# Performance work log

Hardware: AMD Instinct MI355X
Metric: run time of the kernel (lower is better)

## Reference

```python
import jax, jax.numpy as jnp
import numpy as np

V, C, H = 4096, 512, 8
D = C // H
EPS = 1e-5


def setup_inputs():
    key = jax.random.key(0)
    ks = jax.random.split(key, 8)
    s = 0.02
    f32 = jnp.float32
    return {
        "z": jax.random.normal(ks[0], (4, C, 1024), f32),
        "q": 256,
        "codebook": jax.random.normal(ks[1], (V, C), f32) * s,
        "Wq": jax.random.normal(ks[2], (C, C), f32) * s,
        "bq": jnp.zeros((C,), f32),
        "Wk": jax.random.normal(ks[3], (C, C), f32) * s,
        "bk": jnp.zeros((C,), f32),
        "Wv": jax.random.normal(ks[4], (C, C), f32) * s,
        "bv": jnp.zeros((C,), f32),
        "Wp": jax.random.normal(ks[5], (C, H), f32) * s,
        "bp": jnp.zeros((H,), f32),
        "gq": jnp.ones((D,), f32),
        "gk": jnp.ones((D,), f32),
    }


def _rmsnorm(x, g):
    return x * jax.lax.rsqrt(jnp.mean(x * x, axis=-1, keepdims=True) + EPS) * g


def _attn_logits(hs_bct, codebook, Wq, bq, Wk, bk, Wp, bp, gq, gk):
    # pooled cross-attention logits over codebook entries: (B,N,T)
    B, Cc, T = hs_bct.shape
    hs = hs_bct.transpose(0, 2, 1)  # (B,T,C)
    qh = (hs @ Wq + bq).reshape(B, T, H, D).transpose(0, 2, 1, 3)  # (B,H,T,D)
    kh = (codebook @ Wk + bk).reshape(-1, H, D).transpose(1, 0, 2)  # (H,N,D)
    c = hs @ Wp + bp  # (B,T,H) head-pooling weights
    qh = _rmsnorm(qh, gq)
    kh = _rmsnorm(kh, gk)
    logits = jnp.einsum('bhtd,hnd->bhnt', qh, kh) * (1.0 / float(np.sqrt(D)))
    logits = jnp.einsum('bth,bhnt->bnt', c, logits) * (1.0 / float(np.sqrt(H)))
    return logits


def _linear_interp(x, T):
    # x: (B,C,q) -> (B,C,T); matches F.interpolate(mode='linear', align_corners=False)
    q = x.shape[-1]
    pos = (jnp.arange(T, dtype=x.dtype) + 0.5) * (q / T) - 0.5
    pos = jnp.clip(pos, 0.0, q - 1.0)
    i0 = jnp.floor(pos).astype(jnp.int32)
    i1 = jnp.minimum(i0 + 1, q - 1)
    w = (pos - i0.astype(x.dtype))
    return x[..., i0] * (1.0 - w) + x[..., i1] * w


def reference(z, q, codebook, Wq, bq, Wk, bk, Wv, bv, Wp, bp, gq, gk):
    B, Cc, T = z.shape
    # area interpolation T -> q (T % q == 0): non-overlapping window mean
    rest = z.reshape(B, Cc, q, T // q).mean(-1) if q != T else z  # (B,C,q)
    logits = _attn_logits(rest, codebook, Wq, bq, Wk, bk, Wp, bp, gq, gk)  # (B,V,q)
    soft = jax.nn.softmax(logits, axis=1)
    code_idx = jnp.argmax(soft, axis=1)  # (B,q)
    hard = jax.nn.one_hot(code_idx, V, dtype=logits.dtype).transpose(0, 2, 1)  # (B,V,q)
    one_hot = hard - jax.lax.stop_gradient(soft) + soft  # straight-through
    value = codebook @ Wv + bv  # (V,C)
    z_hat = jnp.einsum('bnt,nd->bdt', one_hot, value)  # (B,C,q)
    z_hat = _linear_interp(z_hat, T)  # (B,C,T); phi == identity
    # full-resolution index pass (torch.no_grad) for perplexity (eval path)
    logits_org = jax.lax.stop_gradient(
        _attn_logits(z, codebook, Wq, bq, Wk, bk, Wp, bp, gq, gk))
    code_org = jnp.argmax(logits_org, axis=1).reshape(-1)  # (B*T,)
    counts = jnp.zeros((V,), jnp.float32).at[code_org].add(1.0)
    prob = counts / counts.sum()
    perplexity = jnp.exp(-jnp.sum(prob * jnp.log(prob + 1e-7)))
    return z_hat, perplexity
```

## Files before the change

### kernel.cpp

```cpp
#include <hip/hip_runtime.h>
#include <hip/hip_bf16.h>
#include <cfloat>
#include <math.h>

#define NFULL 4096
#define NPOOL 1024
#define NTOK  5120
#define VDIM  4096

typedef __attribute__((ext_vector_type(8))) short short8;
typedef __attribute__((ext_vector_type(4))) float f4;
typedef unsigned long long u64;

#define MFMA16(a,b,c) __builtin_amdgcn_mfma_f32_16x16x32_bf16((a),(b),(c),0,0,0)

static __device__ __forceinline__ void gl_lds16(const void* g, void* l) {
    __builtin_amdgcn_global_load_lds(
        (const __attribute__((address_space(1))) unsigned int*)g,
        (__attribute__((address_space(3))) unsigned int*)l, 16, 0, 0);
}

#define BGEMM3_CORE(AM, Bt)                                                    \
    int lane = tid & 63, w = tid >> 6, wy = w >> 1, wx = w & 1;                \
    int lm = lane & 15, quad = lane >> 4;                                      \
    int lr8 = lane >> 3;                                                       \
    int kcs = (lane & 7) ^ lr8;                                                \
    int rS = w * 32 + lr8;                                                     \
    const __hip_bfloat16* Ag = (AM) + (mB + rS) * 512 + kcs * 8;               \
    const __hip_bfloat16* Bg = (Bt) + (nB + rS) * 512 + kcs * 8;               \
    __hip_bfloat16* Al = As + (w * 32) * 64 + lane * 8;                        \
    __hip_bfloat16* Bl = Bs + (w * 32) * 64 + lane * 8;                        \
    f4 acc[4][4];                                                              \
    _Pragma("unroll") for (int i = 0; i < 4; ++i)                              \
        _Pragma("unroll") for (int j = 0; j < 4; ++j)                          \
            acc[i][j] = f4{0.f, 0.f, 0.f, 0.f};                                \
    int aswz = lm & 7;                                                         \
    for (int kt = 0; kt < 8; ++kt) {                                           \
        __syncthreads();                                                       \
        _Pragma("unroll") for (int i = 0; i < 4; ++i) {                        \
            gl_lds16(Ag + kt * 64 + i * 8 * 512, Al + i * 8 * 64);             \
            gl_lds16(Bg + kt * 64 + i * 8 * 512, Bl + i * 8 * 64);             \
        }                                                                      \
        __syncthreads();                                                       \
        _Pragma("unroll") for (int s = 0; s < 2; ++s) {                        \
            short8 aF[4], bF[4];                                               \
            int slot = ((s * 4 + quad) ^ aswz) << 3;                           \
            _Pragma("unroll") for (int mt = 0; mt < 4; ++mt)                   \
                aF[mt] = *(const short8*)(As + (wy * 64 + mt * 16 + lm) * 64 + slot); \
            _Pragma("unroll") for (int nt = 0; nt < 4; ++nt)                   \
                bF[nt] = *(const short8*)(Bs + (wx * 64 + nt * 16 + lm) * 64 + slot); \
            _Pragma("unroll") for (int mt = 0; mt < 4; ++mt)                   \
                _Pragma("unroll") for (int nt = 0; nt < 4; ++nt)               \
                    acc[mt][nt] = MFMA16(aF[mt], bF[nt], acc[mt][nt]);         \
        }                                                                      \
    }

__global__ void prep_k(const float* __restrict__ z, const float* __restrict__ cbk,
                       const float* __restrict__ Wq, const float* __restrict__ Wv,
                       float* __restrict__ X, __hip_bfloat16* __restrict__ Xh,
                       __hip_bfloat16* __restrict__ cbh,
                       __hip_bfloat16* __restrict__ WqT, __hip_bfloat16* __restrict__ WvT,
                       u64* __restrict__ packed, unsigned int* __restrict__ Kmax2i) {
    __shared__ float smem[33 * 32];
    int bx = blockIdx.x;
    if (bx < 2048) {
        float (*tile)[33] = (float(*)[33])smem;
        int t0 = (bx & 31) * 32, c0 = ((bx >> 5) & 15) * 32, b = bx >> 9;
        int tx = threadIdx.x & 31, ty = threadIdx.x >> 5;
        #pragma unroll
        for (int i = 0; i < 4; ++i) {
            int c = ty + i * 8;
            tile[c][tx] = z[((b << 9) + c0 + c) * 1024 + t0 + tx];
        }
        __syncthreads();
        #pragma unroll
        for (int i = 0; i < 4; ++i) {
            int tl = ty + i * 8;
            int tok = (b << 10) + t0 + tl;
            Xh[tok * 512 + c0 + tx] = __float2bfloat16(tile[tx][tl]);
        }
        float m = 0.25f * (tile[tx][ty * 4] + tile[tx][ty * 4 + 1] +
                           tile[tx][ty * 4 + 2] + tile[tx][ty * 4 + 3]);
        int tq = (t0 >> 2) + ty;
        X[(NFULL + (b << 8) + tq) * 512 + c0 + tx] = m;
    } else if (bx < 4096) {
        int i0 = (bx - 2048) * 1024 + threadIdx.x * 4;
        float4 v = *(const float4*)(cbk + i0);
        __hip_bfloat16* d = cbh + i0;
        d[0] = __float2bfloat16(v.x); d[1] = __float2bfloat16(v.y);
        d[2] = __float2bfloat16(v.z); d[3] = __float2bfloat16(v.w);
    } else if (bx < 4608) {
        int lin = bx - 4096;
        const float* W = (lin >> 8) ? Wv : Wq;
        __hip_bfloat16* WT = (lin >> 8) ? WvT : WqT;
        float (*t)[33] = (float(*)[33])smem;
        int bk = ((lin >> 4) & 15) * 32, bn = (lin & 15) * 32;
        int lx = threadIdx.x & 31, ly = threadIdx.x >> 5;
        #pragma unroll
        for (int i = 0; i < 4; ++i) {
            int r = ly * 4 + i;
            t[r][lx] = W[(bk + r) * 512 + bn + lx];
        }
        __syncthreads();
        #pragma unroll
        for (int i = 0; i < 4; ++i) {
            int r = ly * 4 + i;
            WT[(bn + r) * 512 + bk + lx] = __float2bfloat16(t[lx][r]);
        }
    } else {
        int i = (bx - 4608) * 256 + threadIdx.x;
        packed[i] = 0ull;
        if (bx == 4608 && threadIdx.x == 0) Kmax2i[0] = 0u;
    }
}

__global__ __launch_bounds__(256) void mid1_k(
    const __hip_bfloat16* __restrict__ Xh,
    const float* __restrict__ cbk, const float* __restrict__ Xp,
    const float* __restrict__ Wk, const float* __restrict__ Wq,
    const float* __restrict__ Wp, const float* __restrict__ bp,
    float* __restrict__ P0, float* __restrict__ P1, float* __restrict__ Cp) {
    __shared__ __align__(16) char smraw[16640];
    int bx = blockIdx.x, tid = threadIdx.x;
    if (bx < 640) {
        float (*As2)[68]  = (float(*)[68])smraw;
        float (*Bs2)[132] = (float(*)[132])(smraw + 16 * 68 * 4);
        int kz = bx >= 320;
        int rem = bx - kz * 320;
        int mB = (rem % 80) * 64, nB = (rem / 80) * 128, kOff = kz * 256;
        const float *A, *B;
        if (mB < NFULL) { A = cbk + mB * 512; B = Wk; }
        else            { A = Xp + (mB - NFULL) * 512; B = Wq; }
        int ty = tid >> 4, tx = tid & 15;
        int arow = tid >> 2, achk = tid & 3;
        int brow = tid >> 4, bcol = (tid & 15) * 4;
        const float* Ap = A + arow * 512 + kOff + achk * 4;
        const float* Bp = B + (kOff + brow) * 512 + nB + bcol;
        float acc[4][8] = {};
        for (int kt = 0; kt < 16; ++kt) {
            float4 a  = *(const float4*)(Ap + kt * 16);
            float4 b0 = *(const float4*)(Bp + kt * 16 * 512);
            float4 b1 = *(const float4*)(Bp + kt * 16 * 512 + 64);
            __syncthreads();
            As2[achk * 4 + 0][arow] = a.x; As2[achk * 4 + 1][arow] = a.y;
            As2[achk * 4 + 2][arow] = a.z; As2[achk * 4 + 3][arow] = a.w;
            *(float4*)&Bs2[brow][bcol]      = b0;
            *(float4*)&Bs2[brow][bcol + 64] = b1;
            __syncthreads();
            #pragma unroll
            for (int kk = 0; kk < 16; ++kk) {
                float4 av  = *(const float4*)&As2[kk][ty * 4];
                float4 bv0 = *(const float4*)&Bs2[kk][tx * 4];
                float4 bv1 = *(const float4*)&Bs2[kk][64 + tx * 4];
                float a4[4] = {av.x, av.y, av.z, av.w};
                float b8[8] = {bv0.x, bv0.y, bv0.z, bv0.w, bv1.x, bv1.y, bv1.z, bv1.w};
                #pragma unroll
                for (int i = 0; i < 4; ++i)
                    #pragma unroll
                    for (int j = 0; j < 8; ++j)
                        acc[i][j] = fmaf(a4[i], b8[j], acc[i][j]);
            }
        }
        float* P = kz ? P1 : P0;
        #pragma unroll
        for (int i = 0; i < 4; ++i) {
            int row = mB + ty * 4 + i;
            float4 r0, r1;
            r0.x = acc[i][0]; r0.y = acc[i][1]; r0.z = acc[i][2]; r0.w = acc[i][3];
            r1.x = acc[i][4]; r1.y = acc[i][5]; r1.z = acc[i][6]; r1.w = acc[i][7];
            *(float4*)&P[row * 512 + nB + tx * 4]      = r0;
            *(float4*)&P[row * 512 + nB + 64 + tx * 4] = r1;
        }
    } else {
        float* Wl = (float*)smraw;
        for (int i = tid; i < 4096; i += 256) Wl[i + (i >> 6)] = Wp[i];
        __syncthreads();
        int w = tid >> 6, lane = tid & 63;
        int tok = (bx - 640) * 4 + w;
        float x[8];
        if (tok < NFULL) {
            short8 xv = *(const short8*)(Xh + tok * 512 + lane * 8);
            #pragma unroll
            for (int j = 0; j < 8; ++j)
                x[j] = __uint_as_float(((unsigned)(unsigned short)xv[j]) << 16);
        } else {
            const float* xp = Xp + (tok - NFULL) * 512 + lane * 8;
            float4 a = *(const float4*)xp, b = *(const float4*)(xp + 4);
            x[0] = a.x; x[1] = a.y; x[2] = a.z; x[3] = a.w;
            x[4] = b.x; x[5] = b.y; x[6] = b.z; x[7] = b.w;
        }
        float s[8] = {};
        int base = lane * 65;
        #pragma unroll
        for (int j = 0; j < 8; ++j)
            #pragma unroll
            for (int h = 0; h < 8; ++h)
                s[h] = fmaf(x[j], Wl[base + j * 8 + h], s[h]);
        #pragma unroll
        for (int h = 0; h < 8; ++h)
            #pragma unroll
            for (int o = 32; o > 0; o >>= 1) s[h] += __shfl_xor(s[h], o);
        if (lane == 0) {
            #pragma unroll
            for (int h = 0; h < 8; ++h) Cp[tok * 8 + h] = s[h] + bp[h];
        }
    }
}

__global__ __launch_bounds__(256) void mid2_k(
    const __hip_bfloat16* __restrict__ Xh, const __hip_bfloat16* __restrict__ WqT,
    const __hip_bfloat16* __restrict__ cbh, const __hip_bfloat16* __restrict__ WvT,
    const float* __restrict__ P0, const float* __restrict__ P1,
    const float* __restrict__ bk, const float* __restrict__ bq,
    const float* __restrict__ gk, const float* __restrict__ gq,
    const float* __restrict__ Cp, const float* __restrict__ bvv,
    __hip_bfloat16* __restrict__ Qh, float* __restrict__ Vb,
    float* __restrict__ Kn, __hip_bfloat16* __restrict__ Kh,
    float* __restrict__ Qpool, unsigned int* __restrict__ Kmax2i) {
    __shared__ __align__(16) char smraw[32768];
    int bx = blockIdx.x, tid = threadIdx.x;
    if (bx < 256) {
        int part = bx >> 7, rem = bx & 127;
        int mB = (rem & 31) * 128, nB = (rem >> 5) * 128;
        const __hip_bfloat16* AM = part ? cbh : Xh;
        const __hip_bfloat16* Bt = part ? WvT : WqT;
        __hip_bfloat16* As = (__hip_bfloat16*)smraw;
        __hip_bfloat16* Bs = As + 128 * 64;
        BGEMM3_CORE(AM, Bt)
        if (part == 0) {
            int h = (rem >> 5) * 2 + wx;
            float bb[4], gg[4];
            #pragma unroll
            for (int nt = 0; nt < 4; ++nt) {
                bb[nt] = bq[h * 64 + nt * 16 + lm];
                gg[nt] = gq[nt * 16 + lm];
            }
            #pragma unroll
            for (int mt = 0; mt < 4; ++mt)
                #pragma unroll
                for (int reg = 0; reg < 4; ++reg) {
                    int tok = mB + wy * 64 + mt * 16 + quad * 4 + reg;
                    float vv[4], ss = 0.f;
                    #pragma unroll
                    for (int nt = 0; nt < 4; ++nt) {
                        vv[nt] = acc[mt][nt][reg] + bb[nt];
                        ss = fmaf(vv[nt], vv[nt], ss);
                    }
                    #pragma unroll
                    for (int off = 1; off < 16; off <<= 1) ss += __shfl_xor(ss, off);
                    float sc = rsqrtf(ss * (1.0f / 64.0f) + 1e-5f) *
                               Cp[tok * 8 + h] * 0.04419417382415922f;
                    #pragma unroll
                    for (int nt = 0; nt < 4; ++nt)
                        Qh[tok * 512 + h * 64 + nt * 16 + lm] =
                            __float2bfloat16(vv[nt] * sc * gg[nt]);
                }
        } else {
            float bb[4];
            #pragma unroll
            for (int nt = 0; nt < 4; ++nt) bb[nt] = bvv[nB + wx * 64 + nt * 16 + lm];
            #pragma unroll
            for (int mt = 0; mt < 4; ++mt)
                #pragma unroll
                for (int reg = 0; reg < 4; ++reg) {
                    int m = mB + wy * 64 + mt * 16 + quad * 4 + reg;
                    #pragma unroll
                    for (int nt = 0; nt < 4; ++nt)
                        Vb[m * 512 + nB + wx * 64 + nt * 16 + lm] =
                            acc[mt][nt][reg] + bb[nt];
                }
        }
    } else {
        int w = tid >> 6, lane = tid & 63;
        int row = (bx - 256) * 4 + w;
        bool isQ = row >= NFULL;
        const float* bias = isQ ? bq : bk;
        const float* g = isQ ? gq : gk;
        int c0 = lane * 8;
        const float* p0 = P0 + row * 512 + c0;
        const float* p1 = P1 + row * 512 + c0;
        float4 a0 = *(const float4*)p0,  a1 = *(const float4*)(p0 + 4);
        float4 d0 = *(const float4*)p1,  d1 = *(const float4*)(p1 + 4);
        float4 e0 = *(const float4*)(bias + c0), e1 = *(const float4*)(bias + c0 + 4);
        int gi = (lane & 7) * 8;
        float4 g0 = *(const float4*)(g + gi), g1 = *(const float4*)(g + gi + 4);
        float v[8];
        v[0] = a0.x + d0.x + e0.x; v[1] = a0.y + d0.y + e0.y;
        v[2] = a0.z + d0.z + e0.z; v[3] = a0.w + d0.w + e0.w;
        v[4] = a1.x + d1.x + e1.x; v[5] = a1.y + d1.y + e1.y;
        v[6] = a1.z + d1.z + e1.z; v[7] = a1.w + d1.w + e1.w;
        float ss = 0.f;
        #pragma unroll
        for (int j = 0; j < 8; ++j) ss = fmaf(v[j], v[j], ss);
        ss += __shfl_xor(ss, 1); ss += __shfl_xor(ss, 2); ss += __shfl_xor(ss, 4);
        float sc = rsqrtf(ss * (1.0f / 64.0f) + 1e-5f);
        float gg[8] = {g0.x, g0.y, g0.z, g0.w, g1.x, g1.y, g1.z, g1.w};
        float o_[8];
        #pragma unroll
        for (int j = 0; j < 8; ++j) o_[j] = v[j] * sc * gg[j];
        if (isQ) {
            float cf = Cp[row * 8 + (lane >> 3)] * 0.04419417382415922f;
            #pragma unroll
            for (int j = 0; j < 8; ++j) o_[j] *= cf;
            float* qp = Qpool + (row - NFULL) * 512 + c0;
            *(float4*)qp       = make_float4(o_[0], o_[1], o_[2], o_[3]);
            *(float4*)(qp + 4) = make_float4(o_[4], o_[5], o_[6], o_[7]);
            __hip_bfloat16 hb[8];
            #pragma unroll
            for (int j = 0; j < 8; ++j) hb[j] = __float2bfloat16(o_[j]);
            *(short8*)(Qh + row * 512 + c0) = *(const short8*)hb;
        } else {
            float* kp = Kn + row * 512 + c0;
            *(float4*)kp       = make_float4(o_[0], o_[1], o_[2], o_[3]);
            *(float4*)(kp + 4) = make_float4(o_[4], o_[5], o_[6], o_[7]);
            __hip_bfloat16 hb[8];
            #pragma unroll
            for (int j = 0; j < 8; ++j) hb[j] = __float2bfloat16(o_[j]);
            *(short8*)(Kh + row * 512 + c0) = *(const short8*)hb;
            float rs = 0.f;
            #pragma unroll
            for (int j = 0; j < 8; ++j) rs = fmaf(o_[j], o_[j], rs);
            #pragma unroll
            for (int o = 32; o > 0; o >>= 1) rs += __shfl_xor(rs, o);
            float* wsum = (float*)smraw;
            if (lane == 0) wsum[w] = rs;
            __syncthreads();
            if (tid == 0) {
                float m01 = fmaxf(wsum[0], wsum[1]);
                float m23 = fmaxf(wsum[2], wsum[3]);
                atomicMax(Kmax2i, __float_as_uint(fmaxf(m01, m23)));
            }
        }
    }
}

__global__ __launch_bounds__(512, 4) void logits_full_k(
    const __hip_bfloat16* __restrict__ Qh, const __hip_bfloat16* __restrict__ Kh,
    u64* __restrict__ packed, __hip_bfloat16* __restrict__ Lp) {
    __shared__ __hip_bfloat16 As[128 * 64];
    __shared__ __hip_bfloat16 Bs[256 * 64];
    int tid = threadIdx.x;
    int mB = blockIdx.x * 128, nB = blockIdx.y * 256;
    int lane = tid & 63, w = tid >> 6;
    int wy = w >> 2, wx = w & 3;
    int lm = lane & 15, quad = lane >> 4;
    int lr8 = lane >> 3;
    int kcs = (lane & 7) ^ lr8;
    const __hip_bfloat16* Ag = Qh + (mB + w * 16 + lr8) * 512 + kcs * 8;
    const __hip_bfloat16* Bg = Kh + (nB + w * 32 + lr8) * 512 + kcs * 8;
    __hip_bfloat16* Al = As + (w * 16) * 64 + lane * 8;
    __hip_bfloat16* Bl = Bs + (w * 32) * 64 + lane * 8;
    f4 acc[4][4];
    #pragma unroll
    for (int i = 0; i < 4; ++i)
        #pragma unroll
        for (int j = 0; j < 4; ++j) acc[i][j] = f4{0.f, 0.f, 0.f, 0.f};
    int aswz = lm & 7;
    for (int kt = 0; kt < 8; ++kt) {
        __syncthreads();
        #pragma unroll
        for (int i = 0; i < 2; ++i)
            gl_lds16(Ag + kt * 64 + i * 8 * 512, Al + i * 8 * 64);
        #pragma unroll
        for (int i = 0; i < 4; ++i)
            gl_lds16(Bg + kt * 64 + i * 8 * 512, Bl + i * 8 * 64);
        __syncthreads();
        #pragma unroll
        for (int s = 0; s < 2; ++s) {
            short8 aF[4], bF[4];
            int slot = ((s * 4 + quad) ^ aswz) << 3;
            #pragma unroll
            for (int mt = 0; mt < 4; ++mt)
                aF[mt] = *(const short8*)(As + (wy * 64 + mt * 16 + lm) * 64 + slot);
            #pragma unroll
            for (int nt = 0; nt < 4; ++nt)
                bF[nt] = *(const short8*)(Bs + (wx * 64 + nt * 16 + lm) * 64 + slot);
            #pragma unroll
            for (int mt = 0; mt < 4; ++mt)
                #pragma unroll
                for (int nt = 0; nt < 4; ++nt)
                    acc[mt][nt] = MFMA16(aF[mt], bF[nt], acc[mt][nt]);
        }
    }
    if (blockIdx.x < 32) {
        #pragma unroll
        for (int mt = 0; mt < 4; ++mt)
            #pragma unroll
            for (int reg = 0; reg < 4; ++reg) {
                float bv = -FLT_MAX; int bi = 0;
                #pragma unroll
                for (int nt = 0; nt < 4; ++nt) {
                    float v = acc[mt][nt][reg];
                    int n = nB + wx * 64 + nt * 16 + lm;
                    if (v > bv) { bv = v; bi = n; }
                }
                #pragma unroll
                for (int off = 1; off < 16; off <<= 1) {
                    float ov = __shfl_xor(bv, off);
                    int oi = __shfl_xor(bi, off);
                    if (ov > bv || (ov == bv && oi < bi)) { bv = ov; bi = oi; }
                }
                if (lm == 0) {
                    unsigned ub = __float_as_uint(bv);
                    ub = (ub & 0x80000000u) ? ~ub : (ub | 0x80000000u);
                    u64 key = ((u64)ub << 32) | (u64)(0xFFFFFFFFu - (unsigned)bi);
                    int tok = mB + wy * 64 + mt * 16 + quad * 4 + reg;
                    atomicMax(&packed[tok], key);
                }
            }
    } else {
        #pragma unroll
        for (int mt = 0; mt < 4; ++mt)
            #pragma unroll
            for (int reg = 0; reg < 4; ++reg) {
                int tok = mB + wy * 64 + mt * 16 + quad * 4 + reg;
                long long base = (long long)(tok - NFULL) * 4096;
                #pragma unroll
                for (int nt = 0; nt < 4; ++nt)
                    Lp[base + nB + wx * 64 + nt * 16 + lm] =
                        __float2bfloat16(acc[mt][nt][reg]);
            }
    }
}

__global__ __launch_bounds__(256) void tail_k(
    const float* __restrict__ Qpool, const float* __restrict__ Kn,
    const __hip_bfloat16* __restrict__ Lp, const unsigned int* __restrict__ Kmax2i,
    const u64* __restrict__ packed, int* __restrict__ codeP,
    float* __restrict__ outPpl) {
    __shared__ int cnt[4096];
    __shared__ float red[4];
    int tid = threadIdx.x;
    if (blockIdx.x < 256) {
        int wid = tid >> 6, lane = tid & 63;
        int tok = blockIdx.x * 4 + wid;
        const float* q = Qpool + tok * 512;
        float4 q0 = *(const float4*)(q + lane * 8);
        float4 q1 = *(const float4*)(q + lane * 8 + 4);
        float qs = q0.x * q0.x + q0.y * q0.y + q0.z * q0.z + q0.w * q0.w +
                   q1.x * q1.x + q1.y * q1.y + q1.z * q1.z + q1.w * q1.w;
        #pragma unroll
        for (int o = 32; o > 0; o >>= 1) qs += __shfl_xor(qs, o);
        float delta = 0.0078125f * sqrtf(qs) * sqrtf(__uint_as_float(*Kmax2i));
        const __hip_bfloat16* row = Lp + (long long)tok * 4096;
        float mx = -FLT_MAX;
        for (int c = 0; c < 64; ++c)
            mx = fmaxf(mx, __bfloat162float(row[c * 64 + lane]));
        #pragma unroll
        for (int o = 32; o > 0; o >>= 1) mx = fmaxf(mx, __shfl_xor(mx, o));
        float thr = mx - delta;
        float bv = -FLT_MAX; int bi = 0;
        for (int c = 0; c < 64; ++c) {
            float v = __bfloat162float(row[c * 64 + lane]);
            u64 mask = __ballot(v >= thr);
            while (mask) {
                int l = __ffsll((long long)mask) - 1;
                mask &= mask - 1;
                int n = c * 64 + l;
                const float* k = Kn + n * 512;
                float4 k0 = *(const float4*)(k + lane * 8);
                float4 k1 = *(const float4*)(k + lane * 8 + 4);
                float d = q0.x * k0.x;
                d = fmaf(q0.y, k0.y, d); d = fmaf(q0.z, k0.z, d); d = fmaf(q0.w, k0.w, d);
                d = fmaf(q1.x, k1.x, d); d = fmaf(q1.y, k1.y, d);
                d = fmaf(q1.z, k1.z, d); d = fmaf(q1.w, k1.w, d);
                #pragma unroll
                for (int o = 32; o > 0; o >>= 1) d += __shfl_xor(d, o);
                if (d > bv) { bv = d; bi = n; }
            }
        }
        if (lane == 0) codeP[tok] = bi;
    } else {
        for (int i = tid; i < 4096; i += 256) cnt[i] = 0;
        __syncthreads();
        for (int i = tid; i < 4096; i += 256) {
            int bi = (int)(0xFFFFFFFFu - (unsigned)(packed[i] & 0xFFFFFFFFu));
            atomicAdd(&cnt[bi], 1);
        }
        __syncthreads();
        float s = 0.f;
        for (int i = tid; i < 4096; i += 256) {
            float p = (float)cnt[i] * (1.0f / 4096.0f);
            s += p * logf(p + 1e-7f);
        }
        #pragma unroll
        for (int o = 32; o > 0; o >>= 1) s += __shfl_xor(s, o);
        if ((tid & 63) == 0) red[tid >> 6] = s;
        __syncthreads();
        if (tid == 0)
            outPpl[0] = expf(-(red[0] + red[1] + red[2] + red[3]));
    }
}

__global__ void zhat_k(const float* __restrict__ Vv, const int* __restrict__ codeP,
                       float* __restrict__ out) {
    int w = (blockIdx.x << 2) + (threadIdx.x >> 6);
    int lane = threadIdx.x & 63;
    int b = w >> 8, j = w & 255;
    const int* cb = codeP + (b << 8);
    const float* rm = Vv + cb[max(j - 1, 0)] * 512;
    const float* r0 = Vv + cb[j] * 512;
    const float* rp = Vv + cb[min(j + 1, 255)] * 512;
    #pragma unroll
    for (int i = 0; i < 8; ++i) {
        int c = i * 64 + lane;
        float vm = rm[c], v0 = r0[c], vp = rp[c];
        float4 o;
        o.x = 0.375f * vm + 0.625f * v0;
        o.y = 0.125f * vm + 0.875f * v0;
        o.z = 0.875f * v0 + 0.125f * vp;
        o.w = 0.625f * v0 + 0.375f * vp;
        *(float4*)&out[(((b << 9) + c) << 10) + (j << 2)] = o;
    }
}

extern "C" void kernel_launch(void* const* d_in, const int* in_sizes, int n_in,
                              void* d_out, int out_size, void* d_ws, size_t ws_size,
                              hipStream_t stream) {
    const float* z   = (const float*)d_in[0];
    const float* cbk = (const float*)d_in[2];
    const float* Wq  = (const float*)d_in[3];
    const float* bq  = (const float*)d_in[4];
    const float* Wk  = (const float*)d_in[5];
    const float* bk  = (const float*)d_in[6];
    const float* Wv  = (const float*)d_in[7];
    const float* bv  = (const float*)d_in[8];
    const float* Wp  = (const float*)d_in[9];
    const float* bp  = (const float*)d_in[10];
    const float* gq  = (const float*)d_in[11];
    const float* gk  = (const float*)d_in[12];
    float* out = (float*)d_out;

    float* X      = (float*)d_ws;
    float* Qpool  = X + 5120 * 512;
    float* Kn     = Qpool + 1024 * 512;
    float* Vb     = Kn + 4096 * 512;
    float* Cp     = Vb + 4096 * 512;
    float* P0     = Cp + 5120 * 8;
    float* P1     = P0 + 5120 * 512;
    u64*   packed = (u64*)(P1 + 5120 * 512);
    unsigned int* Kmax2i = (unsigned int*)(packed + 4096);
    int*   codeP  = (int*)(Kmax2i + 4);
    __hip_bfloat16* Qh  = (__hip_bfloat16*)(codeP + 1024);
    __hip_bfloat16* Kh  = Qh + 5120 * 512;
    __hip_bfloat16* Xh  = Kh + 4096 * 512;
    __hip_bfloat16* cbh = Xh + 4096 * 512;
    __hip_bfloat16* WqT = cbh + 4096 * 512;
    __hip_bfloat16* WvT = WqT + 512 * 512;
    __hip_bfloat16* Lp  = (__hip_bfloat16*)P0;

    prep_k<<<4624, 256, 0, stream>>>(z, cbk, Wq, Wv, X, Xh, cbh, WqT, WvT,
                                     packed, Kmax2i);
    mid1_k<<<1920, 256, 0, stream>>>(Xh, cbk, X + 4096 * 512, Wk, Wq, Wp, bp,
                                     P0, P1, Cp);
    mid2_k<<<1536, 256, 0, stream>>>(Xh, WqT, cbh, WvT, P0, P1, bk, bq, gk, gq,
                                     Cp, bv, Qh, Vb, Kn, Kh, Qpool, Kmax2i);
    logits_full_k<<<dim3(40, 16), 512, 0, stream>>>(Qh, Kh, packed, Lp);
    tail_k<<<257, 256, 0, stream>>>(Qpool, Kn, Lp, Kmax2i, packed, codeP,
                                    out + 4 * 512 * 1024);
    zhat_k<<<256, 256, 0, stream>>>(Vb, codeP, out);
}
```

Measured before the change: 223.7 us.

## Split codebook K projection four ways along K and prefetch tiles in mid1

The fp32 codebook@Wk GEMM in mid1_k moves from a 2-way to a 4-way split-K, so more blocks run with shorter K loops. The extra partials go into reused workspace (Kn and X), and mid2_k adds them back in. The main loop also now register-prefetches the next A/B tile while the current one is computed. The aim is better GPU occupancy and hiding global-load latency, at the cost of extra partial-sum traffic and aliasing risk on the reused buffers: mid2_k reads P2 from Kn and writes Kn in the same rows, and P3 aliases X.

```diff
diff --git a/kernel.cpp b/kernel.cpp
--- a/kernel.cpp
+++ b/kernel.cpp
@@ -119,34 +119,51 @@
     const float* __restrict__ cbk, const float* __restrict__ Xp,
     const float* __restrict__ Wk, const float* __restrict__ Wq,
     const float* __restrict__ Wp, const float* __restrict__ bp,
-    float* __restrict__ P0, float* __restrict__ P1, float* __restrict__ Cp) {
+    float* __restrict__ P0, float* __restrict__ P1,
+    float* __restrict__ P2, float* __restrict__ P3,
+    float* __restrict__ Cp) {
     __shared__ __align__(16) char smraw[16640];
     int bx = blockIdx.x, tid = threadIdx.x;
-    if (bx < 640) {
+    if (bx < 1152) {
         float (*As2)[68]  = (float(*)[68])smraw;
         float (*Bs2)[132] = (float(*)[132])(smraw + 16 * 68 * 4);
-        int kz = bx >= 320;
-        int rem = bx - kz * 320;
-        int mB = (rem % 80) * 64, nB = (rem / 80) * 128, kOff = kz * 256;
-        const float *A, *B;
-        if (mB < NFULL) { A = cbk + mB * 512; B = Wk; }
-        else            { A = Xp + (mB - NFULL) * 512; B = Wq; }
+        const float *A, *B; float* P;
+        int mB, nB, kOff, nkt;
+        if (bx < 1024) {
+            int part = bx >> 8, rem = bx & 255;
+            mB = (rem & 63) * 64; nB = (rem >> 6) * 128;
+            kOff = part * 128; nkt = 8;
+            A = cbk + mB * 512; B = Wk;
+            P = (part == 0) ? P0 : (part == 1) ? P1 : (part == 2) ? P2 : P3;
+        } else {
+            int lin = bx - 1024;
+            int part = lin >> 6, rem = lin & 63;
+            mB = NFULL + (rem & 15) * 64; nB = (rem >> 4) * 128;
+            kOff = part * 256; nkt = 16;
+            A = Xp + (rem & 15) * 64 * 512; B = Wq;
+            P = part ? P1 : P0;
+        }
         int ty = tid >> 4, tx = tid & 15;
         int arow = tid >> 2, achk = tid & 3;
         int brow = tid >> 4, bcol = (tid & 15) * 4;
         const float* Ap = A + arow * 512 + kOff + achk * 4;
         const float* Bp = B + (kOff + brow) * 512 + nB + bcol;
         float acc[4][8] = {};
-        for (int kt = 0; kt < 16; ++kt) {
-            float4 a  = *(const float4*)(Ap + kt * 16);
-            float4 b0 = *(const float4*)(Bp + kt * 16 * 512);
-            float4 b1 = *(const float4*)(Bp + kt * 16 * 512 + 64);
+        float4 a  = *(const float4*)(Ap);
+        float4 b0 = *(const float4*)(Bp);
+        float4 b1 = *(const float4*)(Bp + 64);
+        for (int kt = 0; kt < nkt; ++kt) {
             __syncthreads();
             As2[achk * 4 + 0][arow] = a.x; As2[achk * 4 + 1][arow] = a.y;
             As2[achk * 4 + 2][arow] = a.z; As2[achk * 4 + 3][arow] = a.w;
             *(float4*)&Bs2[brow][bcol]      = b0;
             *(float4*)&Bs2[brow][bcol + 64] = b1;
             __syncthreads();
+            if (kt + 1 < nkt) {
+                a  = *(const float4*)(Ap + (kt + 1) * 16);
+                b0 = *(const float4*)(Bp + (kt + 1) * 16 * 512);
+                b1 = *(const float4*)(Bp + (kt + 1) * 16 * 512 + 64);
+            }
             #pragma unroll
             for (int kk = 0; kk < 16; ++kk) {
                 float4 av  = *(const float4*)&As2[kk][ty * 4];
@@ -161,7 +178,6 @@
                         acc[i][j] = fmaf(a4[i], b8[j], acc[i][j]);
             }
         }
-        float* P = kz ? P1 : P0;
         #pragma unroll
         for (int i = 0; i < 4; ++i) {
             int row = mB + ty * 4 + i;
@@ -176,7 +192,7 @@
         for (int i = tid; i < 4096; i += 256) Wl[i + (i >> 6)] = Wp[i];
         __syncthreads();
         int w = tid >> 6, lane = tid & 63;
-        int tok = (bx - 640) * 4 + w;
+        int tok = (bx - 1152) * 4 + w;
         float x[8];
         if (tok < NFULL) {
             short8 xv = *(const short8*)(Xh + tok * 512 + lane * 8);
@@ -211,11 +227,12 @@
     const __hip_bfloat16* __restrict__ Xh, const __hip_bfloat16* __restrict__ WqT,
     const __hip_bfloat16* __restrict__ cbh, const __hip_bfloat16* __restrict__ WvT,
     const float* __restrict__ P0, const float* __restrict__ P1,
+    const float* P2, const float* __restrict__ P3,
     const float* __restrict__ bk, const float* __restrict__ bq,
     const float* __restrict__ gk, const float* __restrict__ gq,
     const float* __restrict__ Cp, const float* __restrict__ bvv,
     __hip_bfloat16* __restrict__ Qh, float* __restrict__ Vb,
-    float* __restrict__ Kn, __hip_bfloat16* __restrict__ Kh,
+    float* Kn, __hip_bfloat16* __restrict__ Kh,
     float* __restrict__ Qpool, unsigned int* __restrict__ Kmax2i) {
     __shared__ __align__(16) char smraw[32768];
     int bx = blockIdx.x, tid = threadIdx.x;
@@ -289,6 +306,16 @@
         v[2] = a0.z + d0.z + e0.z; v[3] = a0.w + d0.w + e0.w;
         v[4] = a1.x + d1.x + e1.x; v[5] = a1.y + d1.y + e1.y;
         v[6] = a1.z + d1.z + e1.z; v[7] = a1.w + d1.w + e1.w;
+        if (!isQ) {
+            const float* p2 = P2 + row * 512 + c0;
+            const float* p3 = P3 + row * 512 + c0;
+            float4 x0 = *(const float4*)p2, x1 = *(const float4*)(p2 + 4);
+            float4 y0 = *(const float4*)p3, y1 = *(const float4*)(p3 + 4);
+            v[0] += x0.x + y0.x; v[1] += x0.y + y0.y;
+            v[2] += x0.z + y0.z; v[3] += x0.w + y0.w;
+            v[4] += x1.x + y1.x; v[5] += x1.y + y1.y;
+            v[6] += x1.z + y1.z; v[7] += x1.w + y1.w;
+        }
         float ss = 0.f;
         #pragma unroll
         for (int j = 0; j < 8; ++j) ss = fmaf(v[j], v[j], ss);
@@ -548,13 +575,16 @@
     __hip_bfloat16* WqT = cbh + 4096 * 512;
     __hip_bfloat16* WvT = WqT + 512 * 512;
     __hip_bfloat16* Lp  = (__hip_bfloat16*)P0;
+    float* P2 = Kn;
+    float* P3 = X;
 
     prep_k<<<4624, 256, 0, stream>>>(z, cbk, Wq, Wv, X, Xh, cbh, WqT, WvT,
                                      packed, Kmax2i);
-    mid1_k<<<1920, 256, 0, stream>>>(Xh, cbk, X + 4096 * 512, Wk, Wq, Wp, bp,
-                                     P0, P1, Cp);
-    mid2_k<<<1536, 256, 0, stream>>>(Xh, WqT, cbh, WvT, P0, P1, bk, bq, gk, gq,
-                                     Cp, bv, Qh, Vb, Kn, Kh, Qpool, Kmax2i);
+    mid1_k<<<2432, 256, 0, stream>>>(Xh, cbk, X + 4096 * 512, Wk, Wq, Wp, bp,
+                                     P0, P1, P2, P3, Cp);
+    mid2_k<<<1536, 256, 0, stream>>>(Xh, WqT, cbh, WvT, P0, P1, P2, P3,
+                                     bk, bq, gk, gq, Cp, bv,
+                                     Qh, Vb, Kn, Kh, Qpool, Kmax2i);
     logits_full_k<<<dim3(40, 16), 512, 0, stream>>>(Qh, Kh, packed, Lp);
     tail_k<<<257, 256, 0, stream>>>(Qpool, Kn, Lp, Kmax2i, packed, codeP,
                                     out + 4 * 512 * 1024);
```

New measurement: 221.7 us, median of 2. No clear change (-0.9%).

## Replace FP32 SIMT K/Q projection GEMMs with split-bf16 MFMA three-term products

Applied to the files above, without the earlier changes.

The codebook@Wk and pooled-X@Wq projections move from a scalar FP32 FMA GEMM split over K to bf16 MFMA GEMMs. Each FP32 operand is split into bf16 high and low parts, and three partial products (hi*hi, hi*lo, lo*hi) approximate FP32 accuracy. The prep kernel now also writes the hi/lo split and transposed copies of the codebook, pooled X, Wk and Wq. The consumer sums three partial buffers instead of two, which adds extra conversion traffic and a third partial-sum read in exchange for tensor-core throughput.

```diff
diff --git a/kernel.cpp b/kernel.cpp
--- a/kernel.cpp
+++ b/kernel.cpp
@@ -57,9 +57,13 @@
 
 __global__ void prep_k(const float* __restrict__ z, const float* __restrict__ cbk,
                        const float* __restrict__ Wq, const float* __restrict__ Wv,
+                       const float* __restrict__ Wk,
                        float* __restrict__ X, __hip_bfloat16* __restrict__ Xh,
-                       __hip_bfloat16* __restrict__ cbh,
-                       __hip_bfloat16* __restrict__ WqT, __hip_bfloat16* __restrict__ WvT,
+                       __hip_bfloat16* __restrict__ cbh, __hip_bfloat16* __restrict__ cbl,
+                       __hip_bfloat16* __restrict__ Xph, __hip_bfloat16* __restrict__ Xpl,
+                       __hip_bfloat16* __restrict__ WqT, __hip_bfloat16* __restrict__ WqTl,
+                       __hip_bfloat16* __restrict__ WvT,
+                       __hip_bfloat16* __restrict__ WkTh, __hip_bfloat16* __restrict__ WkTl,
                        u64* __restrict__ packed, unsigned int* __restrict__ Kmax2i) {
     __shared__ float smem[33 * 32];
     int bx = blockIdx.x;
@@ -82,17 +86,27 @@
         float m = 0.25f * (tile[tx][ty * 4] + tile[tx][ty * 4 + 1] +
                            tile[tx][ty * 4 + 2] + tile[tx][ty * 4 + 3]);
         int tq = (t0 >> 2) + ty;
-        X[(NFULL + (b << 8) + tq) * 512 + c0 + tx] = m;
+        int prow = (b << 8) + tq;
+        X[(NFULL + prow) * 512 + c0 + tx] = m;
+        __hip_bfloat16 mh = __float2bfloat16(m);
+        Xph[prow * 512 + c0 + tx] = mh;
+        Xpl[prow * 512 + c0 + tx] = __float2bfloat16(m - __bfloat162float(mh));
     } else if (bx < 4096) {
         int i0 = (bx - 2048) * 1024 + threadIdx.x * 4;
         float4 v = *(const float4*)(cbk + i0);
         __hip_bfloat16* d = cbh + i0;
-        d[0] = __float2bfloat16(v.x); d[1] = __float2bfloat16(v.y);
-        d[2] = __float2bfloat16(v.z); d[3] = __float2bfloat16(v.w);
-    } else if (bx < 4608) {
+        __hip_bfloat16* dl = cbl + i0;
+        float vv[4] = {v.x, v.y, v.z, v.w};
+        #pragma unroll
+        for (int j = 0; j < 4; ++j) {
+            __hip_bfloat16 h = __float2bfloat16(vv[j]);
+            d[j] = h;
+            dl[j] = __float2bfloat16(vv[j] - __bfloat162float(h));
+        }
+    } else if (bx < 4864) {
         int lin = bx - 4096;
-        const float* W = (lin >> 8) ? Wv : Wq;
-        __hip_bfloat16* WT = (lin >> 8) ? WvT : WqT;
+        int sel = lin >> 8;
+        const float* W = (sel == 0) ? Wq : (sel == 1) ? Wv : Wk;
         float (*t)[33] = (float(*)[33])smem;
         int bk = ((lin >> 4) & 15) * 32, bn = (lin & 15) * 32;
         int lx = threadIdx.x & 31, ly = threadIdx.x >> 5;
@@ -105,78 +119,74 @@
         #pragma unroll
         for (int i = 0; i < 4; ++i) {
             int r = ly * 4 + i;
-            WT[(bn + r) * 512 + bk + lx] = __float2bfloat16(t[lx][r]);
+            float v = t[lx][r];
+            int idx = (bn + r) * 512 + bk + lx;
+            __hip_bfloat16 h = __float2bfloat16(v);
+            if (sel == 0) {
+                WqT[idx] = h;
+                WqTl[idx] = __float2bfloat16(v - __bfloat162float(h));
+            } else if (sel == 1) {
+                WvT[idx] = h;
+            } else {
+                WkTh[idx] = h;
+                WkTl[idx] = __float2bfloat16(v - __bfloat162float(h));
+            }
         }
     } else {
-        int i = (bx - 4608) * 256 + threadIdx.x;
+        int i = (bx - 4864) * 256 + threadIdx.x;
         packed[i] = 0ull;
-        if (bx == 4608 && threadIdx.x == 0) Kmax2i[0] = 0u;
+        if (bx == 4864 && threadIdx.x == 0) Kmax2i[0] = 0u;
     }
 }
 
 __global__ __launch_bounds__(256) void mid1_k(
     const __hip_bfloat16* __restrict__ Xh,
-    const float* __restrict__ cbk, const float* __restrict__ Xp,
-    const float* __restrict__ Wk, const float* __restrict__ Wq,
+    const __hip_bfloat16* __restrict__ cbh, const __hip_bfloat16* __restrict__ cbl,
+    const __hip_bfloat16* __restrict__ Xph, const __hip_bfloat16* __restrict__ Xpl,
+    const __hip_bfloat16* __restrict__ WkTh, const __hip_bfloat16* __restrict__ WkTl,
+    const __hip_bfloat16* __restrict__ WqT, const __hip_bfloat16* __restrict__ WqTl,
+    const float* __restrict__ Xp,
     const float* __restrict__ Wp, const float* __restrict__ bp,
-    float* __restrict__ P0, float* __restrict__ P1, float* __restrict__ Cp) {
-    __shared__ __align__(16) char smraw[16640];
+    float* __restrict__ P0, float* __restrict__ P1,
+    float* P2, float* P2q,
+    float* __restrict__ Cp) {
+    __shared__ __align__(16) char smraw[32768];
     int bx = blockIdx.x, tid = threadIdx.x;
-    if (bx < 640) {
-        float (*As2)[68]  = (float(*)[68])smraw;
-        float (*Bs2)[132] = (float(*)[132])(smraw + 16 * 68 * 4);
-        int kz = bx >= 320;
-        int rem = bx - kz * 320;
-        int mB = (rem % 80) * 64, nB = (rem / 80) * 128, kOff = kz * 256;
-        const float *A, *B;
-        if (mB < NFULL) { A = cbk + mB * 512; B = Wk; }
-        else            { A = Xp + (mB - NFULL) * 512; B = Wq; }
-        int ty = tid >> 4, tx = tid & 15;
-        int arow = tid >> 2, achk = tid & 3;
-        int brow = tid >> 4, bcol = (tid & 15) * 4;
-        const float* Ap = A + arow * 512 + kOff + achk * 4;
-        const float* Bp = B + (kOff + brow) * 512 + nB + bcol;
-        float acc[4][8] = {};
-        for (int kt = 0; kt < 16; ++kt) {
-            float4 a  = *(const float4*)(Ap + kt * 16);
-            float4 b0 = *(const float4*)(Bp + kt * 16 * 512);
-            float4 b1 = *(const float4*)(Bp + kt * 16 * 512 + 64);
-            __syncthreads();
-            As2[achk * 4 + 0][arow] = a.x; As2[achk * 4 + 1][arow] = a.y;
-            As2[achk * 4 + 2][arow] = a.z; As2[achk * 4 + 3][arow] = a.w;
-            *(float4*)&Bs2[brow][bcol]      = b0;
-            *(float4*)&Bs2[brow][bcol + 64] = b1;
-            __syncthreads();
-            #pragma unroll
-            for (int kk = 0; kk < 16; ++kk) {
-                float4 av  = *(const float4*)&As2[kk][ty * 4];
-                float4 bv0 = *(const float4*)&Bs2[kk][tx * 4];
-                float4 bv1 = *(const float4*)&Bs2[kk][64 + tx * 4];
-                float a4[4] = {av.x, av.y, av.z, av.w};
-                float b8[8] = {bv0.x, bv0.y, bv0.z, bv0.w, bv1.x, bv1.y, bv1.z, bv1.w};
-                #pragma unroll
-                for (int i = 0; i < 4; ++i)
-                    #pragma unroll
-                    for (int j = 0; j < 8; ++j)
-                        acc[i][j] = fmaf(a4[i], b8[j], acc[i][j]);
-            }
-        }
-        float* P = kz ? P1 : P0;
-        #pragma unroll
-        for (int i = 0; i < 4; ++i) {
-            int row = mB + ty * 4 + i;
-            float4 r0, r1;
-            r0.x = acc[i][0]; r0.y = acc[i][1]; r0.z = acc[i][2]; r0.w = acc[i][3];
-            r1.x = acc[i][4]; r1.y = acc[i][5]; r1.z = acc[i][6]; r1.w = acc[i][7];
-            *(float4*)&P[row * 512 + nB + tx * 4]      = r0;
-            *(float4*)&P[row * 512 + nB + 64 + tx * 4] = r1;
-        }
+    if (bx < 480) {
+        const __hip_bfloat16 *AM, *Bt; float* P;
+        int mB, nB;
+        if (bx < 384) {
+            int part = bx >> 7, rem = bx & 127;
+            mB = (rem & 31) * 128; nB = (rem >> 5) * 128;
+            AM = (part == 2) ? cbl : cbh;
+            Bt = (part == 1) ? WkTl : WkTh;
+            P  = (part == 0) ? P0 : (part == 1) ? P1 : P2;
+        } else {
+            int lin = bx - 384;
+            int part = lin >> 5, rem = lin & 31;
+            mB = NFULL + (rem & 7) * 128; nB = (rem >> 3) * 128;
+            AM = ((part == 2) ? Xpl : Xph) - NFULL * 512;
+            Bt = (part == 1) ? WqTl : WqT;
+            P  = (part == 0) ? P0 : (part == 1) ? P1 : P2q;
+        }
+        __hip_bfloat16* As = (__hip_bfloat16*)smraw;
+        __hip_bfloat16* Bs = As + 128 * 64;
+        BGEMM3_CORE(AM, Bt)
+        #pragma unroll
+        for (int mt = 0; mt < 4; ++mt)
+            #pragma unroll
+            for (int reg = 0; reg < 4; ++reg) {
+                int m = mB + wy * 64 + mt * 16 + quad * 4 + reg;
+                #pragma unroll
+                for (int nt = 0; nt < 4; ++nt)
+                    P[m * 512 + nB + wx * 64 + nt * 16 + lm] = acc[mt][nt][reg];
+            }
     } else {
         float* Wl = (float*)smraw;
         for (int i = tid; i < 4096; i += 256) Wl[i + (i >> 6)] = Wp[i];
         __syncthreads();
         int w = tid >> 6, lane = tid & 63;
-        int tok = (bx - 640) * 4 + w;
+        int tok = (bx - 480) * 4 + w;
         float x[8];
         if (tok < NFULL) {
             short8 xv = *(const short8*)(Xh + tok * 512 + lane * 8);
@@ -211,12 +221,13 @@
     const __hip_bfloat16* __restrict__ Xh, const __hip_bfloat16* __restrict__ WqT,
     const __hip_bfloat16* __restrict__ cbh, const __hip_bfloat16* __restrict__ WvT,
     const float* __restrict__ P0, const float* __restrict__ P1,
+    const float* P2, const float* P2q,
     const float* __restrict__ bk, const float* __restrict__ bq,
     const float* __restrict__ gk, const float* __restrict__ gq,
     const float* __restrict__ Cp, const float* __restrict__ bvv,
     __hip_bfloat16* __restrict__ Qh, float* __restrict__ Vb,
-    float* __restrict__ Kn, __hip_bfloat16* __restrict__ Kh,
-    float* __restrict__ Qpool, unsigned int* __restrict__ Kmax2i) {
+    float* Kn, __hip_bfloat16* __restrict__ Kh,
+    float* Qpool, unsigned int* __restrict__ Kmax2i) {
     __shared__ __align__(16) char smraw[32768];
     int bx = blockIdx.x, tid = threadIdx.x;
     if (bx < 256) {
@@ -279,16 +290,18 @@
         int c0 = lane * 8;
         const float* p0 = P0 + row * 512 + c0;
         const float* p1 = P1 + row * 512 + c0;
+        const float* p2 = (isQ ? P2q : P2) + row * 512 + c0;
         float4 a0 = *(const float4*)p0,  a1 = *(const float4*)(p0 + 4);
         float4 d0 = *(const float4*)p1,  d1 = *(const float4*)(p1 + 4);
+        float4 x0 = *(const float4*)p2,  x1 = *(const float4*)(p2 + 4);
         float4 e0 = *(const float4*)(bias + c0), e1 = *(const float4*)(bias + c0 + 4);
         int gi = (lane & 7) * 8;
         float4 g0 = *(const float4*)(g + gi), g1 = *(const float4*)(g + gi + 4);
         float v[8];
-        v[0] = a0.x + d0.x + e0.x; v[1] = a0.y + d0.y + e0.y;
-        v[2] = a0.z + d0.z + e0.z; v[3] = a0.w + d0.w + e0.w;
-        v[4] = a1.x + d1.x + e1.x; v[5] = a1.y + d1.y + e1.y;
-        v[6] = a1.z + d1.z + e1.z; v[7] = a1.w + d1.w + e1.w;
+        v[0] = a0.x + d0.x + x0.x + e0.x; v[1] = a0.y + d0.y + x0.y + e0.y;
+        v[2] = a0.z + d0.z + x0.z + e0.z; v[3] = a0.w + d0.w + x0.w + e0.w;
+        v[4] = a1.x + d1.x + x1.x + e1.x; v[5] = a1.y + d1.y + x1.y + e1.y;
+        v[6] = a1.z + d1.z + x1.z + e1.z; v[7] = a1.w + d1.w + x1.w + e1.w;
         float ss = 0.f;
         #pragma unroll
         for (int j = 0; j < 8; ++j) ss = fmaf(v[j], v[j], ss);
@@ -548,13 +561,24 @@
     __hip_bfloat16* WqT = cbh + 4096 * 512;
     __hip_bfloat16* WvT = WqT + 512 * 512;
     __hip_bfloat16* Lp  = (__hip_bfloat16*)P0;
-
-    prep_k<<<4624, 256, 0, stream>>>(z, cbk, Wq, Wv, X, Xh, cbh, WqT, WvT,
+    __hip_bfloat16* cbl  = (__hip_bfloat16*)X;
+    __hip_bfloat16* Xph  = cbl + 4096 * 512;
+    __hip_bfloat16* Xpl  = Xph + 1024 * 512;
+    __hip_bfloat16* WkTh = Xpl + 1024 * 512;
+    __hip_bfloat16* WkTl = WkTh + 512 * 512;
+    __hip_bfloat16* WqTl = WkTl + 512 * 512;
+    float* P2  = Kn;
+    float* P2q = Qpool - NFULL * 512;
+
+    prep_k<<<4880, 256, 0, stream>>>(z, cbk, Wq, Wv, Wk, X, Xh, cbh, cbl,
+                                     Xph, Xpl, WqT, WqTl, WvT, WkTh, WkTl,
                                      packed, Kmax2i);
-    mid1_k<<<1920, 256, 0, stream>>>(Xh, cbk, X + 4096 * 512, Wk, Wq, Wp, bp,
-                                     P0, P1, Cp);
-    mid2_k<<<1536, 256, 0, stream>>>(Xh, WqT, cbh, WvT, P0, P1, bk, bq, gk, gq,
-                                     Cp, bv, Qh, Vb, Kn, Kh, Qpool, Kmax2i);
+    mid1_k<<<1760, 256, 0, stream>>>(Xh, cbh, cbl, Xph, Xpl, WkTh, WkTl,
+                                     WqT, WqTl, X + 4096 * 512, Wp, bp,
+                                     P0, P1, P2, P2q, Cp);
+    mid2_k<<<1536, 256, 0, stream>>>(Xh, WqT, cbh, WvT, P0, P1, P2, P2q,
+                                     bk, bq, gk, gq, Cp, bv,
+                                     Qh, Vb, Kn, Kh, Qpool, Kmax2i);
     logits_full_k<<<dim3(40, 16), 512, 0, stream>>>(Qh, Kh, packed, Lp);
     tail_k<<<257, 256, 0, stream>>>(Qpool, Kn, Lp, Kmax2i, packed, codeP,
                                     out + 4 * 512 * 1024);
```

Measured after the change: 202.3 us. -9.6%, faster.
